# Performance work log

Measured on AMD Instinct MI355X. Metric: run time of the kernel, lower is better.

## Reference

```python
import jax, jax.numpy as jnp
import numpy as np

B, N = 16, 300000          # batch, total anchors per image (all FPN levels concatenated)
PRE, POST = 2000, 1000     # num_pre_nms, num_post_nms
NMS_THR = 0.7
MIN_SIZE = 1e-3            # proposal_min_size
IMG_H, IMG_W = 800.0, 1333.0


def setup_inputs() -> dict:
    key = jax.random.key(0)
    k1, k2, k3, k4, k5, k6 = jax.random.split(key, 6)
    cls = jax.random.normal(k1, (B, N), dtype=jnp.float32)
    reg = jax.random.normal(k2, (B, N, 4), dtype=jnp.float32) * 0.1
    # anchors as valid (cx,cy,w,h)->(x1,y1,x2,y2) boxes inside the image
    cx = jax.random.uniform(k3, (B, N), dtype=jnp.float32, minval=0.0, maxval=IMG_W)
    cy = jax.random.uniform(k4, (B, N), dtype=jnp.float32, minval=0.0, maxval=IMG_H)
    w = jax.random.uniform(k5, (B, N), dtype=jnp.float32, minval=16.0, maxval=256.0)
    h = jax.random.uniform(k6, (B, N), dtype=jnp.float32, minval=16.0, maxval=256.0)
    anchors = jnp.stack([cx - 0.5 * w, cy - 0.5 * h, cx + 0.5 * w, cy + 0.5 * h], axis=-1)
    return {"cls": cls, "reg": reg, "anchors": anchors}


def _decode(anchor, reg):
    aw = anchor[:, 2] - anchor[:, 0]
    ah = anchor[:, 3] - anchor[:, 1]
    acx = anchor[:, 0] + 0.5 * aw
    acy = anchor[:, 1] + 0.5 * ah
    dx, dy, dw, dh = reg[:, 0], reg[:, 1], reg[:, 2], reg[:, 3]
    pcx = dx * aw + acx
    pcy = dy * ah + acy
    pw = jnp.exp(dw) * aw
    ph = jnp.exp(dh) * ah
    return jnp.stack([pcx - 0.5 * pw, pcy - 0.5 * ph, pcx + 0.5 * pw, pcy + 0.5 * ph], axis=-1)


def _iou_matrix(boxes):
    # boxes: [K,4] -> pairwise IoU [K,K]
    area = (boxes[:, 2] - boxes[:, 0]) * (boxes[:, 3] - boxes[:, 1])
    lt = jnp.maximum(boxes[:, None, :2], boxes[None, :, :2])
    rb = jnp.minimum(boxes[:, None, 2:], boxes[None, :, 2:])
    wh = jnp.clip(rb - lt, 0.0)
    inter = wh[..., 0] * wh[..., 1]
    union = area[:, None] + area[None, :] - inter
    return inter / jnp.maximum(union, 1e-8)


def _per_image(score, reg, anchor):
    # topk pre-NMS selection (lax.top_k returns score-descending order)
    top_s, idx = jax.lax.top_k(score, PRE)
    boxes = _decode(anchor[idx], reg[idx].reshape(-1, 4))
    # clip to image bounds
    bounds = jnp.array([IMG_W, IMG_H, IMG_W, IMG_H], dtype=boxes.dtype)
    boxes = jnp.clip(boxes, 0.0, bounds)
    # remove small boxes (mask instead of dynamic removal)
    w = boxes[:, 2] - boxes[:, 0]
    h = boxes[:, 3] - boxes[:, 1]
    valid = (w >= MIN_SIZE) & (h >= MIN_SIZE)
    s = jnp.where(valid, top_s, -jnp.inf)
    order = jnp.argsort(-s)  # score-descending, invalid last
    boxes = boxes[order]
    valid = valid[order]
    # greedy NMS: iterate highest-score-first, suppress later boxes with IoU > thr
    iou = _iou_matrix(boxes)
    rng = jnp.arange(PRE)
    def body(i, keep):
        sup = (iou[i] > NMS_THR) & keep[i]
        return keep & jnp.logical_not(sup & (rng > i))
    keep = jax.lax.fori_loop(0, PRE, body, valid)
    # gather kept boxes (score order preserved), pad with zeros past count
    sel = jnp.argsort(jnp.logical_not(keep), stable=True)[:POST]
    return boxes[sel] * keep[sel][:, None].astype(boxes.dtype)


def reference(cls, reg, anchors):
    # [B, POST, 4] proposals per image (zero-padded where fewer than POST kept)
    return jax.vmap(_per_image)(cls, reg, anchors)
```

## Files before the change

kernel.cpp:

```cpp
#include <hip/hip_runtime.h>

#define NB 16
#define NN 300000
#define PRE 2000
#define POST 1000

typedef unsigned long long ull;

static const size_t OFF_HIST1   = 0;
static const size_t OFF_HIST2   = 65536;
static const size_t OFF_HIST3   = 196608;
static const size_t OFF_CANDCNT = 327680;
static const size_t OFF_EQCNT   = 327936;
static const size_t OFF_BITMAP  = 328192;
static const size_t OFF_B1      = 332288;
static const size_t OFF_NEED1   = 332544;
static const size_t OFF_B2      = 332800;
static const size_t OFF_NEED2   = 333056;
static const size_t OFF_B3      = 333312;
static const size_t OFF_NEED3   = 333568;
static const size_t OFF_NVALID  = 333824;
static const size_t ZERO_BYTES  = 334080;
static const size_t OFF_CAND    = 334080;
static const size_t OFF_EQBUF   = 465152;
static const size_t OFF_KEYS    = 989440;
static const size_t OFF_BOXTMP  = 1251584;
static const size_t OFF_SORTED  = 1775872;
static const size_t OFF_MASK    = 2287872;

__device__ __forceinline__ unsigned f2u(float f){
  unsigned b = __float_as_uint(f);
  return (b & 0x80000000u) ? ~b : (b | 0x80000000u);
}

#define H1REP 8
#define H1STRIDE 1025
__global__ void k_hist1(const float* __restrict__ cls, unsigned* __restrict__ hist){
  __shared__ unsigned h[H1REP * H1STRIDE];
  int img = blockIdx.y;
  for (int i = threadIdx.x; i < H1REP * H1STRIDE; i += blockDim.x) h[i] = 0;
  __syncthreads();
  const float* p = cls + (size_t)img * NN;
  int stride = gridDim.x * blockDim.x;
  unsigned rep = (threadIdx.x & (H1REP - 1)) * H1STRIDE;
  for (int i = blockIdx.x * blockDim.x + threadIdx.x; i < NN; i += stride)
    atomicAdd(&h[rep + (f2u(p[i]) >> 22)], 1u);
  __syncthreads();
  unsigned* g = hist + img * 1024;
  for (int i = threadIdx.x; i < 1024; i += blockDim.x){
    unsigned v = 0;
    for (int r = 0; r < H1REP; r++) v += h[r * H1STRIDE + i];
    if (v) atomicAdd(&g[i], v);
  }
}

__global__ void k_scan(const unsigned* __restrict__ hist, int bins,
                       const unsigned* __restrict__ tgt, unsigned K0,
                       unsigned* __restrict__ outBin, unsigned* __restrict__ outNeed){
  int img = blockIdx.x;
  int t = threadIdx.x;
  const unsigned* hh = hist + img * bins;
  unsigned K = tgt ? tgt[img] : K0;
  int per = bins >> 8;
  unsigned s = 0;
  for (int q = 0; q < per; q++) s += hh[bins - 1 - (t * per + q)];
  __shared__ unsigned arr[256];
  arr[t] = s;
  __syncthreads();
  for (int off = 1; off < 256; off <<= 1){
    unsigned v = (t >= off) ? arr[t - off] : 0u;
    __syncthreads();
    arr[t] += v;
    __syncthreads();
  }
  unsigned incl = arr[t], excl = incl - s;
  if (excl < K && K <= incl){
    unsigned c = excl;
    for (int q = 0; q < per; q++){
      int b = bins - 1 - (t * per + q);
      unsigned cnt = hh[b];
      if (c + cnt >= K){ outBin[img] = (unsigned)b; outNeed[img] = K - c; break; }
      c += cnt;
    }
  }
}

__global__ void k_hist2(const float* __restrict__ cls, const unsigned* __restrict__ b1,
                        unsigned* __restrict__ hist){
  int img = blockIdx.y;
  unsigned bb1 = b1[img];
  const float* p = cls + (size_t)img * NN;
  unsigned* g = hist + img * 2048;
  int stride = gridDim.x * blockDim.x;
  for (int i = blockIdx.x * blockDim.x + threadIdx.x; i < NN; i += stride){
    unsigned u = f2u(p[i]);
    if ((u >> 22) == bb1) atomicAdd(&g[(u >> 11) & 0x7FFu], 1u);
  }
}

__global__ void k_hist3(const float* __restrict__ cls, const unsigned* __restrict__ b1,
                        const unsigned* __restrict__ b2, unsigned* __restrict__ hist){
  int img = blockIdx.y;
  unsigned pref = (b1[img] << 11) | b2[img];
  const float* p = cls + (size_t)img * NN;
  unsigned* g = hist + img * 2048;
  int stride = gridDim.x * blockDim.x;
  for (int i = blockIdx.x * blockDim.x + threadIdx.x; i < NN; i += stride){
    unsigned u = f2u(p[i]);
    if ((u >> 11) == pref) atomicAdd(&g[u & 0x7FFu], 1u);
  }
}

__global__ void k_compact(const float* __restrict__ cls, const unsigned* __restrict__ b1,
                          const unsigned* __restrict__ b2, const unsigned* __restrict__ b3,
                          unsigned* __restrict__ cand, unsigned* __restrict__ candCnt,
                          unsigned* __restrict__ eqbuf, unsigned* __restrict__ eqCnt){
  __shared__ unsigned lc[1024];
  __shared__ unsigned le[256];
  __shared__ unsigned lcn, len_, baseC, baseE;
  int img = blockIdx.y;
  if (threadIdx.x == 0){ lcn = 0; len_ = 0; }
  __syncthreads();
  unsigned T = (b1[img] << 22) | (b2[img] << 11) | b3[img];
  const float* p = cls + (size_t)img * NN;
  int stride = gridDim.x * blockDim.x;
  for (int i = blockIdx.x * blockDim.x + threadIdx.x; i < NN; i += stride){
    unsigned u = f2u(p[i]);
    if (u > T){
      unsigned pos = atomicAdd(&lcn, 1u);
      if (pos < 1024u) lc[pos] = (unsigned)i;
      else { unsigned g = atomicAdd(&candCnt[img], 1u); if (g < 2048u) cand[img * 2048 + g] = (unsigned)i; }
    } else if (u == T){
      unsigned pos = atomicAdd(&len_, 1u);
      if (pos < 256u) le[pos] = (unsigned)i;
      else { unsigned g = atomicAdd(&eqCnt[img], 1u); if (g < 8192u) eqbuf[img * 8192 + g] = (unsigned)i; }
    }
  }
  __syncthreads();
  unsigned nc = lcn < 1024u ? lcn : 1024u;
  unsigned ne = len_ < 256u ? len_ : 256u;
  if (threadIdx.x == 0){
    if (nc) baseC = atomicAdd(&candCnt[img], nc);
    if (ne) baseE = atomicAdd(&eqCnt[img], ne);
  }
  __syncthreads();
  for (unsigned t = threadIdx.x; t < nc; t += blockDim.x){
    unsigned g = baseC + t;
    if (g < 2048u) cand[img * 2048 + g] = lc[t];
  }
  for (unsigned t = threadIdx.x; t < ne; t += blockDim.x){
    unsigned g = baseE + t;
    if (g < 8192u) eqbuf[img * 8192 + g] = le[t];
  }
}

__global__ void k_finalize(unsigned* __restrict__ cand, const unsigned* __restrict__ candCnt,
                           const unsigned* __restrict__ eqbuf, const unsigned* __restrict__ eqCnt,
                           const unsigned* __restrict__ need3){
  int img = blockIdx.x, tid = threadIdx.x;
  unsigned need = need3[img];
  unsigned ec = eqCnt[img]; if (ec > 8192u) ec = 8192u;
  unsigned base = candCnt[img];
  const unsigned* eq = eqbuf + img * 8192;
  unsigned* c = cand + img * 2048;
  if (need >= ec){
    for (unsigned t = tid; t < ec; t += 256) if (base + t < 2048u) c[base + t] = eq[t];
    return;
  }
  for (unsigned t = tid; t < ec; t += 256){
    unsigned v = eq[t], r = 0;
    for (unsigned s = 0; s < ec; s++) r += (eq[s] < v) ? 1u : 0u;
    if (r < need && base + r < 2048u) c[base + r] = v;
  }
}

__global__ void k_decode(const float* __restrict__ cls, const float* __restrict__ reg,
                         const float* __restrict__ anch, const unsigned* __restrict__ cand,
                         float* __restrict__ boxTmp, ull* __restrict__ keys,
                         unsigned* __restrict__ nvalid){
  int s = blockIdx.x * blockDim.x + threadIdx.x;
  if (s >= NB * 2048) return;
  int img = s >> 11, slot = s & 2047;
  ull key = 0ull;
  float4 box = make_float4(0.f, 0.f, 0.f, 0.f);
  bool counted = false;
  if (slot < PRE){
    unsigned i = cand[img * 2048 + slot];
    if (i < NN){
      size_t gi = (size_t)img * NN + i;
      float4 a = ((const float4*)anch)[gi];
      float4 r = ((const float4*)reg)[gi];
      float sc = cls[gi];
      float aw = a.z - a.x, ah = a.w - a.y;
      float acx = a.x + 0.5f * aw, acy = a.y + 0.5f * ah;
      float pcx = r.x * aw + acx, pcy = r.y * ah + acy;
      float pw = expf(r.z) * aw, ph = expf(r.w) * ah;
      float x1 = pcx - 0.5f * pw, y1 = pcy - 0.5f * ph;
      float x2 = pcx + 0.5f * pw, y2 = pcy + 0.5f * ph;
      x1 = fminf(fmaxf(x1, 0.f), 1333.f); x2 = fminf(fmaxf(x2, 0.f), 1333.f);
      y1 = fminf(fmaxf(y1, 0.f), 800.f);  y2 = fminf(fmaxf(y2, 0.f), 800.f);
      bool valid = ((x2 - x1) >= 0.001f) && ((y2 - y1) >= 0.001f);
      unsigned up = valid ? f2u(sc) : 0u;
      key = ((ull)up << 32) | (ull)(0xFFFFFFFFu - i);
      box = make_float4(x1, y1, x2, y2);
      counted = valid;
    }
  }
  keys[img * 2048 + slot] = key;
  ((float4*)boxTmp)[img * 2048 + slot] = box;
  ull bal = __ballot(counted);
  if ((threadIdx.x & 63) == 0 && bal)
    atomicAdd(&nvalid[img], (unsigned)__popcll(bal));
}

__global__ __launch_bounds__(256) void k_rank(const ull* __restrict__ keys,
                                              const float* __restrict__ boxTmp,
                                              float* __restrict__ sorted){
  __shared__ ull lk[2048];
  int img = blockIdx.y;
  int e = blockIdx.x * 256 + threadIdx.x;
  for (int t = threadIdx.x; t < 2048; t += 256) lk[t] = keys[img * 2048 + t];
  __syncthreads();
  ull me = lk[e];
  unsigned rank = 0;
  #pragma unroll 8
  for (int j = 0; j < 2048; j++) rank += (lk[j] > me) ? 1u : 0u;
  if (rank < PRE)
    ((float4*)sorted)[img * PRE + rank] = ((const float4*)boxTmp)[img * 2048 + e];
}

__global__ __launch_bounds__(512) void k_mask(const float* __restrict__ sorted,
                                              const unsigned* __restrict__ nvalid,
                                              ull* __restrict__ mask, ull* __restrict__ bitmap){
  __shared__ float4 bx[PRE];
  __shared__ float  ar[PRE];
  __shared__ unsigned rowflag[16];
  int img = blockIdx.y, tid = threadIdx.x;
  if (tid < 16) rowflag[tid] = 0;
  for (int i = tid; i < PRE; i += 512){
    float4 b = ((const float4*)sorted)[img * PRE + i];
    bx[i] = b;
    ar[i] = (b.z - b.x) * (b.w - b.y);
  }
  __syncthreads();
  int row = blockIdx.x * 16 + (tid >> 5);
  int w = tid & 31;
  float4 bi = bx[row];
  float ai = ar[row];
  int qlo = (row >= w) ? (((row - w) >> 5) + 1) : 0;
  int qhi = ((PRE - 1 - w) >> 5) + 1;
  ull m = 0;
  for (int q = qlo; q < qhi; q++){
    int j = (q << 5) + w;
    float4 bj = bx[j];
    float xx1 = fmaxf(bi.x, bj.x), yy1 = fmaxf(bi.y, bj.y);
    float xx2 = fminf(bi.z, bj.z), yy2 = fminf(bi.w, bj.w);
    float ww = fmaxf(xx2 - xx1, 0.f), hh = fmaxf(yy2 - yy1, 0.f);
    float inter = ww * hh;
    float uni = ai + ar[j] - inter;
    if (inter / fmaxf(uni, 1e-8f) > 0.7f) m |= (1ull << q);
  }
  mask[((size_t)(img * PRE + row)) * 32 + w] = m;
  if (m) atomicOr(&rowflag[tid >> 5], 1u);
  __syncthreads();
  if (tid < 16){
    int r = blockIdx.x * 16 + tid;
    if (rowflag[tid] && r < (int)nvalid[img])
      atomicOr(&bitmap[img * 32 + (r >> 6)], 1ull << (r & 63));
  }
}

__global__ __launch_bounds__(256) void k_nms(const ull* __restrict__ mask,
                                             const ull* __restrict__ bitmap,
                                             const unsigned* __restrict__ nvalid,
                                             const float* __restrict__ sorted,
                                             float* __restrict__ out){
  __shared__ unsigned rows[2048];
  __shared__ int mcount;
  __shared__ ull cache[192 * 32];
  __shared__ ull keepP[32];
  __shared__ ull keepLin[32];
  __shared__ unsigned cntArr[32], preArr[32];
  int img = blockIdx.x, tid = threadIdx.x;
  int lane = tid & 63, wave = tid >> 6;
  if (tid == 0){
    int m = 0;
    for (int w0 = 0; w0 < 32; w0++){
      ull bits = bitmap[img * 32 + w0];
      while (bits){
        int b = __ffsll(bits) - 1;
        rows[m++] = (unsigned)(w0 * 64 + b);
        bits &= bits - 1;
      }
    }
    mcount = m;
  }
  __syncthreads();
  int m = mcount;
  ull remv = 0;
  for (int base = 0; base < m; base += 192){
    int cnt = min(192, m - base);
    for (int t = tid; t < cnt * 32; t += 256){
      unsigned rr = rows[base + (t >> 5)];
      cache[t] = mask[((size_t)(img * PRE + rr)) * 32 + (t & 31)];
    }
    __syncthreads();
    if (wave == 0){
      for (int q = 0; q < cnt; q++){
        int i = (int)rows[base + q];
        int wi = i & 31, bi = i >> 5;
        int sup = (lane == wi) && ((remv >> bi) & 1ull);
        if (!__any(sup)){
          if (lane < 32) remv |= cache[(q << 5) + lane];
        }
      }
    }
    __syncthreads();
  }
  int nv = (int)nvalid[img];
  if (wave == 0 && lane < 32){
    int cnt2 = (nv > lane) ? (((nv - 1 - lane) >> 5) + 1) : 0;
    ull vm = (cnt2 >= 64) ? ~0ull : ((1ull << cnt2) - 1ull);
    keepP[lane] = (~remv) & vm;
  }
  __syncthreads();
  if (tid < 32){
    ull lin = 0;
    for (int kk = 0; kk < 64; kk++)
      lin |= ((keepP[kk & 31] >> (2 * tid + (kk >> 5))) & 1ull) << kk;
    keepLin[tid] = lin;
    cntArr[tid] = (unsigned)__popcll(lin);
  }
  __syncthreads();
  if (tid < 32){
    unsigned pre = 0;
    for (int w0 = 0; w0 < tid; w0++) pre += cntArr[w0];
    preArr[tid] = pre;
  }
  __syncthreads();
  for (int i = tid; i < PRE; i += 256){
    int w0 = i >> 6, b = i & 63;
    ull kw = keepLin[w0];
    if ((kw >> b) & 1ull){
      unsigned rank = preArr[w0] + (unsigned)__popcll(kw & ((1ull << b) - 1ull));
      if (rank < POST)
        ((float4*)out)[img * POST + rank] = ((const float4*)sorted)[img * PRE + i];
    }
  }
}

extern "C" void kernel_launch(void* const* d_in, const int* in_sizes, int n_in,
                              void* d_out, int out_size, void* d_ws, size_t ws_size,
                              hipStream_t stream){
  const float* cls  = (const float*)d_in[0];
  const float* reg  = (const float*)d_in[1];
  const float* anch = (const float*)d_in[2];
  float* out = (float*)d_out;
  char* ws = (char*)d_ws;

  unsigned* hist1   = (unsigned*)(ws + OFF_HIST1);
  unsigned* hist2   = (unsigned*)(ws + OFF_HIST2);
  unsigned* hist3   = (unsigned*)(ws + OFF_HIST3);
  unsigned* candCnt = (unsigned*)(ws + OFF_CANDCNT);
  unsigned* eqCnt   = (unsigned*)(ws + OFF_EQCNT);
  ull*      bitmap  = (ull*)     (ws + OFF_BITMAP);
  unsigned* b1      = (unsigned*)(ws + OFF_B1);
  unsigned* need1   = (unsigned*)(ws + OFF_NEED1);
  unsigned* b2      = (unsigned*)(ws + OFF_B2);
  unsigned* need2   = (unsigned*)(ws + OFF_NEED2);
  unsigned* b3      = (unsigned*)(ws + OFF_B3);
  unsigned* need3   = (unsigned*)(ws + OFF_NEED3);
  unsigned* nvalid  = (unsigned*)(ws + OFF_NVALID);
  unsigned* cand    = (unsigned*)(ws + OFF_CAND);
  unsigned* eqbuf   = (unsigned*)(ws + OFF_EQBUF);
  ull*      keys    = (ull*)     (ws + OFF_KEYS);
  float*    boxTmp  = (float*)   (ws + OFF_BOXTMP);
  float*    sorted  = (float*)   (ws + OFF_SORTED);
  ull*      mask    = (ull*)     (ws + OFF_MASK);

  hipMemsetAsync(ws, 0, ZERO_BYTES, stream);
  hipMemsetAsync(d_out, 0, (size_t)out_size * sizeof(float), stream);

  k_hist1<<<dim3(64, NB), 256, 0, stream>>>(cls, hist1);
  k_scan <<<NB, 256, 0, stream>>>(hist1, 1024, (const unsigned*)nullptr, 2000u, b1, need1);
  k_hist2<<<dim3(64, NB), 256, 0, stream>>>(cls, b1, hist2);
  k_scan <<<NB, 256, 0, stream>>>(hist2, 2048, need1, 0u, b2, need2);
  k_hist3<<<dim3(64, NB), 256, 0, stream>>>(cls, b1, b2, hist3);
  k_scan <<<NB, 256, 0, stream>>>(hist3, 2048, need2, 0u, b3, need3);
  k_compact<<<dim3(64, NB), 256, 0, stream>>>(cls, b1, b2, b3, cand, candCnt, eqbuf, eqCnt);
  k_finalize<<<NB, 256, 0, stream>>>(cand, candCnt, eqbuf, eqCnt, need3);
  k_decode<<<(NB * 2048) / 256, 256, 0, stream>>>(cls, reg, anch, cand, boxTmp, keys, nvalid);
  k_rank<<<dim3(8, NB), 256, 0, stream>>>(keys, boxTmp, sorted);
  k_mask<<<dim3(PRE / 16, NB), 512, 0, stream>>>(sorted, nvalid, mask, bitmap);
  k_nms<<<NB, 256, 0, stream>>>(mask, bitmap, nvalid, sorted, out);
}
```

Before: 335.1 us.

## Double-buffer NMS mask rows with producer waves and parallelize row list build

The NMS kernel now splits work between waves: waves 1-3 prefetch the next 48-row chunk of suppression masks into a second LDS buffer while wave 0 runs the serial greedy scan on the current chunk. Wave 0 also register-prefetches the row ids and mask words eight at a time to hide LDS latency. The compacted list of rows that have overlaps is built in parallel from per-word popcounts instead of by one thread. The list is padded to a multiple of 48 with row PRE-1, which relies on that row's mask being harmless. The padding also adds extra iterations to the serial loop.

```diff
diff --git a/kernel.cpp b/kernel.cpp
--- a/kernel.cpp
+++ b/kernel.cpp
@@ -270,53 +270,116 @@
   }
 }
 
+#define CHR 48
 __global__ __launch_bounds__(256) void k_nms(const ull* __restrict__ mask,
                                              const ull* __restrict__ bitmap,
                                              const unsigned* __restrict__ nvalid,
                                              const float* __restrict__ sorted,
                                              float* __restrict__ out){
-  __shared__ unsigned rows[2048];
-  __shared__ int mcount;
-  __shared__ ull cache[192 * 32];
+  __shared__ unsigned rowsLds[2048];
+  __shared__ unsigned cntw[32];
+  __shared__ unsigned wbaseS[32];
+  __shared__ int mcountS, mpS;
+  __shared__ ull cacheD[2][CHR * 32];
   __shared__ ull keepP[32];
   __shared__ ull keepLin[32];
   __shared__ unsigned cntArr[32], preArr[32];
   int img = blockIdx.x, tid = threadIdx.x;
   int lane = tid & 63, wave = tid >> 6;
+
+  if (tid < 32) cntw[tid] = (unsigned)__popcll(bitmap[img * 32 + tid]);
+  __syncthreads();
   if (tid == 0){
-    int m = 0;
-    for (int w0 = 0; w0 < 32; w0++){
-      ull bits = bitmap[img * 32 + w0];
-      while (bits){
-        int b = __ffsll(bits) - 1;
-        rows[m++] = (unsigned)(w0 * 64 + b);
-        bits &= bits - 1;
+    unsigned s = 0;
+    for (int w0 = 0; w0 < 32; w0++){ wbaseS[w0] = s; s += cntw[w0]; }
+    mcountS = (int)s;
+    mpS = ((int)s + CHR - 1) / CHR * CHR;
+  }
+  __syncthreads();
+  int m = mcountS, mp = mpS;
+  if (tid < 32){
+    ull bits = bitmap[img * 32 + tid];
+    unsigned pos = wbaseS[tid];
+    int base_i = tid * 64;
+    while (bits){
+      int b = __ffsll((long long)bits) - 1;
+      rowsLds[pos++] = (unsigned)(base_i + b);
+      bits &= bits - 1;
+    }
+  }
+  for (int t = m + tid; t < mp; t += 256) rowsLds[t] = PRE - 1;
+  __syncthreads();
+
+  int nch = mp / CHR;
+  ull remv = 0;
+  const ull* mg = mask + (size_t)img * PRE * 32;
+
+  if (nch > 0 && tid >= 64){
+    int s = tid - 64;
+    ull v[8];
+    #pragma unroll
+    for (int k = 0; k < 8; k++){
+      int t = k * 192 + s;
+      unsigned rr = rowsLds[t >> 5];
+      v[k] = mg[(size_t)rr * 32 + (t & 31)];
+    }
+    #pragma unroll
+    for (int k = 0; k < 8; k++) cacheD[0][k * 192 + s] = v[k];
+  }
+  __syncthreads();
+
+  for (int c = 0; c < nch; c++){
+    int cb = c & 1;
+    if (tid >= 64){
+      if (c + 1 < nch){
+        int q0n = (c + 1) * CHR;
+        int s = tid - 64;
+        ull v[8];
+        #pragma unroll
+        for (int k = 0; k < 8; k++){
+          int t = k * 192 + s;
+          unsigned rr = rowsLds[q0n + (t >> 5)];
+          v[k] = mg[(size_t)rr * 32 + (t & 31)];
+        }
+        #pragma unroll
+        for (int k = 0; k < 8; k++) cacheD[cb ^ 1][k * 192 + s] = v[k];
       }
-    }
-    mcount = m;
-  }
-  __syncthreads();
-  int m = mcount;
-  ull remv = 0;
-  for (int base = 0; base < m; base += 192){
-    int cnt = min(192, m - base);
-    for (int t = tid; t < cnt * 32; t += 256){
-      unsigned rr = rows[base + (t >> 5)];
-      cache[t] = mask[((size_t)(img * PRE + rr)) * 32 + (t & 31)];
-    }
-    __syncthreads();
-    if (wave == 0){
-      for (int q = 0; q < cnt; q++){
-        int i = (int)rows[base + q];
-        int wi = i & 31, bi = i >> 5;
-        int sup = (lane == wi) && ((remv >> bi) & 1ull);
-        if (!__any(sup)){
-          if (lane < 32) remv |= cache[(q << 5) + lane];
+    } else {
+      const ull* cbuf = cacheD[cb];
+      const int q0 = c * CHR;
+      ull cur[8]; unsigned ci[8];
+      #pragma unroll
+      for (int k = 0; k < 8; k++){
+        ci[k] = rowsLds[q0 + k];
+        cur[k] = cbuf[(k << 5) | (lane & 31)];
+      }
+      #pragma unroll
+      for (int g = 0; g < 6; g++){
+        ull nxt[8]; unsigned ni[8];
+        if (g < 5){
+          #pragma unroll
+          for (int k = 0; k < 8; k++){
+            int lq = (g + 1) * 8 + k;
+            ni[k] = rowsLds[q0 + lq];
+            nxt[k] = cbuf[(lq << 5) | (lane & 31)];
+          }
+        }
+        #pragma unroll
+        for (int k = 0; k < 8; k++){
+          unsigned i = ci[k];
+          unsigned bit = ((unsigned)(remv >> (i >> 5))) & 1u;
+          int sup = (lane == (int)(i & 31)) && bit;
+          if (!__any(sup)) remv |= cur[k];
+        }
+        if (g < 5){
+          #pragma unroll
+          for (int k = 0; k < 8; k++){ cur[k] = nxt[k]; ci[k] = ni[k]; }
         }
       }
     }
     __syncthreads();
   }
+
   int nv = (int)nvalid[img];
   if (wave == 0 && lane < 32){
     int cnt2 = (nv > lane) ? (((nv - 1 - lane) >> 5) + 1) : 0;
```

Result: faster. 305.3 us (-8.9%).
